# Optimization experiments

Hardware: AMD Instinct MI355X
Metric: run time of the kernel (lower is better)

Reference implementation:

```python
import jax, jax.numpy as jnp
import numpy as np

B, N, T, D, H = 8, 1000, 64, 32, 4
HD = D // H
GEN_INTERVAL = 5.0


def setup_inputs() -> dict:
    key = jax.random.key(0)
    ks = jax.random.split(key, 10)
    s = 1.0 / np.sqrt(D)
    inp = {
        "x": jax.random.normal(ks[0], (B, N, T, D), dtype=jnp.float32),
        "q_w": jax.random.uniform(ks[1], (D, D), jnp.float32, -s, s),
        "q_b": jnp.zeros((D,), jnp.float32),
        "k_w": jax.random.uniform(ks[2], (D, D), jnp.float32, -s, s),
        "k_b": jnp.zeros((D,), jnp.float32),
        "v_w": jax.random.uniform(ks[3], (D, D), jnp.float32, -s, s),
        "v_b": jnp.zeros((D,), jnp.float32),
        "out_w": jax.random.uniform(ks[4], (D, D), jnp.float32, -s, s),
        "out_b": jnp.zeros((D,), jnp.float32),
        "rel_pos_bias": jax.random.uniform(ks[5], (H, T, T), jnp.float32, -s, s),
        "log_gi": jnp.array(np.log(GEN_INTERVAL), jnp.float32),
    }
    return inp


def _gi_mask(log_gi, t):
    # generation-interval weighting: gaussian around gen_int + recency term, causal
    gen_int = jnp.exp(log_gi)
    times = jnp.arange(t, dtype=jnp.float32)
    lag = times[:, None] - times[None, :]  # [T, T]
    weight = jnp.exp(-0.5 * ((lag - gen_int) / (gen_int * 0.5)) ** 2)
    recent = jnp.exp(-0.1 * jnp.abs(lag))
    mask = 0.7 * weight + 0.3 * recent
    causal = jnp.tril(jnp.ones((t, t), jnp.float32))
    return mask * causal


def reference(x, q_w, q_b, k_w, k_b, v_w, v_b, out_w, out_b, rel_pos_bias, log_gi):
    b, n, t, d = x.shape
    xf = x.reshape(b * n, t, d)
    q = (xf @ q_w + q_b).reshape(b * n, t, H, HD).transpose(0, 2, 1, 3)  # [BN,H,T,hd]
    k = (xf @ k_w + k_b).reshape(b * n, t, H, HD).transpose(0, 2, 1, 3)
    v = (xf @ v_w + v_b).reshape(b * n, t, H, HD).transpose(0, 2, 1, 3)
    scale = jnp.sqrt(jnp.asarray(HD, jnp.float32))
    attn = jnp.einsum("bhqd,bhkd->bhqk", q, k) / scale  # [BN,H,T,T]
    attn = attn + rel_pos_bias[None]
    gi = _gi_mask(log_gi, t)
    attn = attn * gi[None, None]
    attn = jax.nn.softmax(attn, axis=-1)
    out = jnp.einsum("bhqk,bhkd->bhqd", attn, v)
    out = out.transpose(0, 2, 1, 3).reshape(b * n, t, d)
    out = out @ out_w + out_b
    return out.reshape(b, n, t, d)
```

## Files before the change

kernel.cpp:

```cpp
#include <hip/hip_runtime.h>
#include <math.h>

namespace {
constexpr int T_ = 64;
constexpr int D_ = 32;

typedef _Float16 half2 __attribute__((ext_vector_type(2)));
typedef _Float16 half4 __attribute__((ext_vector_type(4)));
typedef _Float16 half8 __attribute__((ext_vector_type(8)));
typedef float f32x4 __attribute__((ext_vector_type(4)));

union H4 { half4 v4; half2 v2[2]; };

__global__ __launch_bounds__(256) void gia_prep(
    const float* __restrict__ qw, const float* __restrict__ kw,
    const float* __restrict__ vw, const float* __restrict__ ow,
    const float* __restrict__ rel, const float* __restrict__ lgi,
    float* __restrict__ gis32, _Float16* __restrict__ ebg,
    _Float16* __restrict__ wimg)
{
    int t = blockIdx.x * 256 + threadIdx.x;
    const float gv = __expf(lgi[0]);
    const float LOG2E = 1.4426950408889634f;
    const float INVS  = 0.35355339059327373f;
    if (t < 1024) {
        int nt = t >> 8, mt = (t >> 6) & 3, lane = t & 63;
        int q  = (lane & 15) + 16 * nt;
        int k0 = 16 * mt + 4 * (lane >> 4);
#pragma unroll
        for (int r = 0; r < 4; ++r) {
            int k = k0 + r;
            float gi = 0.0f;
            if (k <= q) {
                float lag = (float)(q - k);
                float z = (lag - gv) / (0.5f * gv);
                gi = 0.7f * __expf(-0.5f * z * z) + 0.3f * __expf(-0.1f * lag);
            }
            gis32[t * 4 + r] = gi * INVS * LOG2E;
        }
    } else if (t < 5120) {
        int e = t - 1024;
        int h = e >> 10, nt = (e >> 8) & 3, mt = (e >> 6) & 3, lane = e & 63;
        int q  = (lane & 15) + 16 * nt;
        int k0 = 16 * mt + 4 * (lane >> 4);
#pragma unroll
        for (int r = 0; r < 4; ++r) {
            int k = k0 + r;
            float gi = 0.0f;
            if (k <= q) {
                float lag = (float)(q - k);
                float z = (lag - gv) / (0.5f * gv);
                gi = 0.7f * __expf(-0.5f * z * z) + 0.3f * __expf(-0.1f * lag);
            }
            ebg[e * 4 + r] = (_Float16)__expf(rel[(h * 64 + q) * 64 + k] * gi);
        }
    } else if (t < 7424) {
        int wi = t - 5120;
        const float* wp[4] = {qw, kw, vw, ow};
#pragma unroll
        for (int e = 0; e < 2; ++e) {
            int flat = wi * 2 + e;
            int m = flat / 1152, rem = flat % 1152;
            int c2 = rem / 36, kk = rem % 36;
            float v = (kk < 32) ? wp[m][kk * 32 + c2] : 0.0f;
            wimg[flat] = (_Float16)v;
        }
    }
}

__global__ __launch_bounds__(256) void gia_main(
    const float* __restrict__ x,
    const float* __restrict__ qb_, const float* __restrict__ kb_,
    const float* __restrict__ vb_, const float* __restrict__ ob_,
    const float* __restrict__ gis32, const _Float16* __restrict__ ebg,
    const _Float16* __restrict__ wimg,
    float* __restrict__ out)
{
    __shared__ __align__(16) _Float16 xs[64][40];
    __shared__ __align__(16) _Float16 wS[4][32][36];
    __shared__ __align__(16) _Float16 qs[64][40];
    __shared__ __align__(16) _Float16 ks_[64][40];
    __shared__ __align__(16) _Float16 vT[37][72];
    __shared__ float bS[4][32];
    __shared__ float invS[4][64];

    const int tid  = threadIdx.x;
    const int lane = tid & 63;
    const int w    = tid >> 6;
    const int l4   = lane & 15;
    const int g    = lane >> 4;
    const int bn   = blockIdx.x;

    {
        const float4* xv = (const float4*)(x + (size_t)bn * 2048);
        float4 a = xv[2 * tid], b = xv[2 * tid + 1];
        int t = tid >> 2, c = (tid & 3) * 8;
        half8 hx;
        hx[0] = (_Float16)a.x; hx[1] = (_Float16)a.y;
        hx[2] = (_Float16)a.z; hx[3] = (_Float16)a.w;
        hx[4] = (_Float16)b.x; hx[5] = (_Float16)b.y;
        hx[6] = (_Float16)b.z; hx[7] = (_Float16)b.w;
        *(half8*)&xs[t][c] = hx;

        const uint4* wsrc = (const uint4*)wimg;
        uint4* wdst = (uint4*)&wS[0][0][0];
        wdst[tid]       = wsrc[tid];
        wdst[tid + 256] = wsrc[tid + 256];
        if (tid < 64) wdst[tid + 512] = wsrc[tid + 512];

        if (tid < 128) {
            int h = tid >> 5, j = tid & 31;
            half2 o2 = {(_Float16)1.0f, (_Float16)1.0f};
            *(half2*)&vT[9 * h + 8][2 * j] = o2;
        }
        if (tid < 128) {
            int m = tid >> 5, i = tid & 31;
            const float* bp = (m == 0) ? qb_ : (m == 1) ? kb_ : (m == 2) ? vb_ : ob_;
            bS[m][i] = bp[i];
        }
    }
    __syncthreads();

    {
        half4 xa0 = *(const half4*)&xs[16 * w + l4][4 * g];
        half4 xa1 = *(const half4*)&xs[16 * w + l4][4 * g + 16];
#pragma unroll
        for (int m = 0; m < 3; ++m) {
#pragma unroll
            for (int nt = 0; nt < 2; ++nt) {
                half4 wb0 = *(const half4*)&wS[m][l4 + 16 * nt][4 * g];
                half4 wb1 = *(const half4*)&wS[m][l4 + 16 * nt][4 * g + 16];
                f32x4 acc = {};
                acc = __builtin_amdgcn_mfma_f32_16x16x16f16(xa0, wb0, acc, 0, 0, 0);
                acc = __builtin_amdgcn_mfma_f32_16x16x16f16(xa1, wb1, acc, 0, 0, 0);
                float bb = bS[m][l4 + 16 * nt];
                if (m == 0) {
#pragma unroll
                    for (int r = 0; r < 4; ++r)
                        qs[g * 4 + r + 16 * w][l4 + 16 * nt] = (_Float16)(acc[r] + bb);
                } else if (m == 1) {
#pragma unroll
                    for (int r = 0; r < 4; ++r)
                        ks_[g * 4 + r + 16 * w][l4 + 16 * nt] = (_Float16)(acc[r] + bb);
                } else {
                    half4 pv;
#pragma unroll
                    for (int r = 0; r < 4; ++r) pv[r] = (_Float16)(acc[r] + bb);
                    int c = l4 + 16 * nt;
                    *(half4*)&vT[9 * (c >> 3) + (c & 7)][g * 4 + 16 * w] = pv;
                }
            }
        }
    }
    __syncthreads();

    {
        const int h = w;
        half4 kfr[4], qfr[4], vfr[4];
#pragma unroll
        for (int mt = 0; mt < 4; ++mt) {
            half4 v = {};
            if (g < 2) v = *(const half4*)&ks_[l4 + 16 * mt][8 * h + 4 * g];
            kfr[mt] = v;
        }
#pragma unroll
        for (int nt = 0; nt < 4; ++nt) {
            half4 v = {};
            if (g < 2) v = *(const half4*)&qs[l4 + 16 * nt][8 * h + 4 * g];
            qfr[nt] = v;
        }
        const int vrow = 9 * h + (l4 < 9 ? l4 : 9);
#pragma unroll
        for (int ks = 0; ks < 4; ++ks)
            vfr[ks] = *(const half4*)&vT[vrow][4 * g + 16 * ks];

        f32x4 oacc[4];
#pragma unroll
        for (int i = 0; i < 4; ++i) oacc[i] = (f32x4){};

#pragma unroll
        for (int nt = 0; nt < 4; ++nt) {
            f32x4 s[4];
#pragma unroll
            for (int mt = 0; mt < 4; ++mt) {
                f32x4 z = {};
                s[mt] = __builtin_amdgcn_mfma_f32_16x16x16f16(kfr[mt], qfr[nt], z, 0, 0, 0);
            }
            half4 af[4];
#pragma unroll
            for (int mt = 0; mt < 4; ++mt) {
                f32x4 g4 = *(const f32x4*)&gis32[((nt * 4 + mt) * 64 + lane) * 4];
                half4 eb = *(const half4*)&ebg[(((h * 4 + nt) * 4 + mt) * 64 + lane) * 4];
                float t0 = s[mt][0] * g4[0];
                float t1 = s[mt][1] * g4[1];
                float t2 = s[mt][2] * g4[2];
                float t3 = s[mt][3] * g4[3];
                H4 u;
                u.v2[0] = __builtin_bit_cast(half2, __builtin_amdgcn_cvt_pkrtz(exp2f(t0), exp2f(t1)));
                u.v2[1] = __builtin_bit_cast(half2, __builtin_amdgcn_cvt_pkrtz(exp2f(t2), exp2f(t3)));
                af[mt] = u.v4 * eb;
            }
#pragma unroll
            for (int ks = 0; ks < 4; ++ks)
                oacc[nt] = __builtin_amdgcn_mfma_f32_16x16x16f16(af[ks], vfr[ks], oacc[nt], 0, 0, 0);
        }

        _Float16 (*os_)[40] = xs;
        if (l4 < 8) {
#pragma unroll
            for (int nt = 0; nt < 4; ++nt)
#pragma unroll
                for (int r = 0; r < 4; ++r)
                    os_[g * 4 + r + 16 * nt][8 * h + l4] = (_Float16)oacc[nt][r];
        } else if (l4 == 8) {
#pragma unroll
            for (int nt = 0; nt < 4; ++nt)
#pragma unroll
                for (int r = 0; r < 4; ++r)
                    invS[h][g * 4 + r + 16 * nt] = oacc[nt][r];
        }
    }
    __syncthreads();

    {
        _Float16 (*os_)[40] = xs;
        half4 oa0 = *(const half4*)&os_[16 * w + l4][4 * g];
        half4 oa1 = *(const half4*)&os_[16 * w + l4][4 * g + 16];
        float i0 = 1.0f / invS[g >> 1][16 * w + l4];
        float i1 = 1.0f / invS[2 + (g >> 1)][16 * w + l4];
        _Float16 h0 = (_Float16)i0, h1 = (_Float16)i1;
        oa0 *= (half4){h0, h0, h0, h0};
        oa1 *= (half4){h1, h1, h1, h1};
        float* yout = out + (size_t)bn * 2048;
#pragma unroll
        for (int nt = 0; nt < 2; ++nt) {
            half4 wb0 = *(const half4*)&wS[3][l4 + 16 * nt][4 * g];
            half4 wb1 = *(const half4*)&wS[3][l4 + 16 * nt][4 * g + 16];
            f32x4 y = {};
            y = __builtin_amdgcn_mfma_f32_16x16x16f16(oa0, wb0, y, 0, 0, 0);
            y = __builtin_amdgcn_mfma_f32_16x16x16f16(oa1, wb1, y, 0, 0, 0);
            float bb = bS[3][l4 + 16 * nt];
#pragma unroll
            for (int r = 0; r < 4; ++r)
                yout[(g * 4 + r + 16 * w) * 32 + l4 + 16 * nt] = y[r] + bb;
        }
    }
}

}

extern "C" void kernel_launch(void* const* d_in, const int* in_sizes, int n_in,
                              void* d_out, int out_size, void* d_ws, size_t ws_size,
                              hipStream_t stream)
{
    const float* x   = (const float*)d_in[0];
    const float* qw  = (const float*)d_in[1];
    const float* qb  = (const float*)d_in[2];
    const float* kw  = (const float*)d_in[3];
    const float* kb  = (const float*)d_in[4];
    const float* vw  = (const float*)d_in[5];
    const float* vb  = (const float*)d_in[6];
    const float* ow  = (const float*)d_in[7];
    const float* ob  = (const float*)d_in[8];
    const float* rel = (const float*)d_in[9];
    const float* lgi = (const float*)d_in[10];
    float* outp = (float*)d_out;

    float*    gis32 = (float*)d_ws;
    _Float16* ebg   = (_Float16*)((char*)d_ws + 16384);
    _Float16* wimg  = (_Float16*)((char*)d_ws + 49152);

    const int bn_count = in_sizes[0] / (T_ * D_);

    gia_prep<<<dim3(29), dim3(256), 0, stream>>>(qw, kw, vw, ow, rel, lgi,
                                                 gis32, ebg, wimg);
    gia_main<<<dim3(bn_count), dim3(256), 0, stream>>>(
        x, qb, kb, vb, ob, gis32, ebg, wimg, outp);
}
```

Measured before the change: 66.14 us.

## Use 16x16x32 MFMA, fold bias into exp2 FMA, shrink LDS for occupancy

Replaces pairs of 16x16x16 f16 MFMAs with single 16x16x32 MFMAs for the projections and output GEMM. The relative-position bias is now precomputed in log2 space as fp32 and fused into the exponent via an FMA, removing the per-element fp16 multiply. The output-projection weights and bias move into registers, shared arrays are trimmed, and launch bounds request 6 blocks per SM. Together these aim to cut LDS footprint and instruction count so more blocks stay resident. The cost is a doubled bias table in global memory and more register pressure.

```diff
diff --git a/kernel.cpp b/kernel.cpp
--- a/kernel.cpp
+++ b/kernel.cpp
@@ -11,12 +11,13 @@
 typedef float f32x4 __attribute__((ext_vector_type(4)));
 
 union H4 { half4 v4; half2 v2[2]; };
+union H8 { half8 v8; half4 v4[2]; };
 
 __global__ __launch_bounds__(256) void gia_prep(
     const float* __restrict__ qw, const float* __restrict__ kw,
     const float* __restrict__ vw, const float* __restrict__ ow,
     const float* __restrict__ rel, const float* __restrict__ lgi,
-    float* __restrict__ gis32, _Float16* __restrict__ ebg,
+    float* __restrict__ gis32, float* __restrict__ lb32,
     _Float16* __restrict__ wimg)
 {
     int t = blockIdx.x * 256 + threadIdx.x;
@@ -52,7 +53,7 @@
                 float z = (lag - gv) / (0.5f * gv);
                 gi = 0.7f * __expf(-0.5f * z * z) + 0.3f * __expf(-0.1f * lag);
             }
-            ebg[e * 4 + r] = (_Float16)__expf(rel[(h * 64 + q) * 64 + k] * gi);
+            lb32[e * 4 + r] = rel[(h * 64 + q) * 64 + k] * gi * LOG2E;
         }
     } else if (t < 7424) {
         int wi = t - 5120;
@@ -68,21 +69,21 @@
     }
 }
 
-__global__ __launch_bounds__(256) void gia_main(
+__global__ __launch_bounds__(256, 6) void gia_main(
     const float* __restrict__ x,
     const float* __restrict__ qb_, const float* __restrict__ kb_,
     const float* __restrict__ vb_, const float* __restrict__ ob_,
-    const float* __restrict__ gis32, const _Float16* __restrict__ ebg,
+    const float* __restrict__ gis32, const float* __restrict__ lb32,
     const _Float16* __restrict__ wimg,
     float* __restrict__ out)
 {
     __shared__ __align__(16) _Float16 xs[64][40];
-    __shared__ __align__(16) _Float16 wS[4][32][36];
-    __shared__ __align__(16) _Float16 qs[64][40];
-    __shared__ __align__(16) _Float16 ks_[64][40];
-    __shared__ __align__(16) _Float16 vT[37][72];
-    __shared__ float bS[4][32];
-    __shared__ float invS[4][64];
+    __shared__ __align__(16) _Float16 wS[3][32][36];
+    __shared__ __align__(16) _Float16 qs[64][36];
+    __shared__ __align__(16) _Float16 ks_[64][36];
+    __shared__ __align__(16) _Float16 vT[36][68];
+    __shared__ float bS[3][32];
+    __shared__ _Float16 invS[4][64];
 
     const int tid  = threadIdx.x;
     const int lane = tid & 63;
@@ -90,6 +91,15 @@
     const int l4   = lane & 15;
     const int g    = lane >> 4;
     const int bn   = blockIdx.x;
+
+    H8 wo[2]; float obv[2];
+#pragma unroll
+    for (int nt = 0; nt < 2; ++nt) {
+        const _Float16* wp = wimg + 3 * 1152 + (l4 + 16 * nt) * 36 + 8 * g;
+        wo[nt].v4[0] = *(const half4*)wp;
+        wo[nt].v4[1] = *(const half4*)(wp + 4);
+        obv[nt] = ob_[l4 + 16 * nt];
+    }
 
     {
         const float4* xv = (const float4*)(x + (size_t)bn * 2048);
@@ -104,35 +114,33 @@
 
         const uint4* wsrc = (const uint4*)wimg;
         uint4* wdst = (uint4*)&wS[0][0][0];
-        wdst[tid]       = wsrc[tid];
-        wdst[tid + 256] = wsrc[tid + 256];
-        if (tid < 64) wdst[tid + 512] = wsrc[tid + 512];
+        wdst[tid] = wsrc[tid];
+        if (tid < 176) wdst[tid + 256] = wsrc[tid + 256];
 
         if (tid < 128) {
             int h = tid >> 5, j = tid & 31;
             half2 o2 = {(_Float16)1.0f, (_Float16)1.0f};
             *(half2*)&vT[9 * h + 8][2 * j] = o2;
         }
-        if (tid < 128) {
+        if (tid < 96) {
             int m = tid >> 5, i = tid & 31;
-            const float* bp = (m == 0) ? qb_ : (m == 1) ? kb_ : (m == 2) ? vb_ : ob_;
+            const float* bp = (m == 0) ? qb_ : (m == 1) ? kb_ : vb_;
             bS[m][i] = bp[i];
         }
     }
     __syncthreads();
 
     {
-        half4 xa0 = *(const half4*)&xs[16 * w + l4][4 * g];
-        half4 xa1 = *(const half4*)&xs[16 * w + l4][4 * g + 16];
+        half8 xa = *(const half8*)&xs[16 * w + l4][8 * g];
 #pragma unroll
         for (int m = 0; m < 3; ++m) {
 #pragma unroll
             for (int nt = 0; nt < 2; ++nt) {
-                half4 wb0 = *(const half4*)&wS[m][l4 + 16 * nt][4 * g];
-                half4 wb1 = *(const half4*)&wS[m][l4 + 16 * nt][4 * g + 16];
+                H8 wb;
+                wb.v4[0] = *(const half4*)&wS[m][l4 + 16 * nt][8 * g];
+                wb.v4[1] = *(const half4*)&wS[m][l4 + 16 * nt][8 * g + 4];
                 f32x4 acc = {};
-                acc = __builtin_amdgcn_mfma_f32_16x16x16f16(xa0, wb0, acc, 0, 0, 0);
-                acc = __builtin_amdgcn_mfma_f32_16x16x16f16(xa1, wb1, acc, 0, 0, 0);
+                acc = __builtin_amdgcn_mfma_f32_16x16x32_f16(xa, wb.v8, acc, 0, 0, 0);
                 float bb = bS[m][l4 + 16 * nt];
                 if (m == 0) {
 #pragma unroll
@@ -169,7 +177,7 @@
             if (g < 2) v = *(const half4*)&qs[l4 + 16 * nt][8 * h + 4 * g];
             qfr[nt] = v;
         }
-        const int vrow = 9 * h + (l4 < 9 ? l4 : 9);
+        const int vrow = 9 * h + (l4 < 9 ? l4 : 8);
 #pragma unroll
         for (int ks = 0; ks < 4; ++ks)
             vfr[ks] = *(const half4*)&vT[vrow][4 * g + 16 * ks];
@@ -189,16 +197,16 @@
             half4 af[4];
 #pragma unroll
             for (int mt = 0; mt < 4; ++mt) {
-                f32x4 g4 = *(const f32x4*)&gis32[((nt * 4 + mt) * 64 + lane) * 4];
-                half4 eb = *(const half4*)&ebg[(((h * 4 + nt) * 4 + mt) * 64 + lane) * 4];
-                float t0 = s[mt][0] * g4[0];
-                float t1 = s[mt][1] * g4[1];
-                float t2 = s[mt][2] * g4[2];
-                float t3 = s[mt][3] * g4[3];
+                f32x4 g4  = *(const f32x4*)&gis32[((nt * 4 + mt) * 64 + lane) * 4];
+                f32x4 lbv = *(const f32x4*)&lb32[(((h * 4 + nt) * 4 + mt) * 64 + lane) * 4];
+                float t0 = fmaf(s[mt][0], g4[0], lbv[0]);
+                float t1 = fmaf(s[mt][1], g4[1], lbv[1]);
+                float t2 = fmaf(s[mt][2], g4[2], lbv[2]);
+                float t3 = fmaf(s[mt][3], g4[3], lbv[3]);
                 H4 u;
                 u.v2[0] = __builtin_bit_cast(half2, __builtin_amdgcn_cvt_pkrtz(exp2f(t0), exp2f(t1)));
                 u.v2[1] = __builtin_bit_cast(half2, __builtin_amdgcn_cvt_pkrtz(exp2f(t2), exp2f(t3)));
-                af[mt] = u.v4 * eb;
+                af[mt] = u.v4;
             }
 #pragma unroll
             for (int ks = 0; ks < 4; ++ks)
@@ -217,32 +225,28 @@
             for (int nt = 0; nt < 4; ++nt)
 #pragma unroll
                 for (int r = 0; r < 4; ++r)
-                    invS[h][g * 4 + r + 16 * nt] = oacc[nt][r];
+                    invS[h][g * 4 + r + 16 * nt] = (_Float16)oacc[nt][r];
         }
     }
     __syncthreads();
 
     {
         _Float16 (*os_)[40] = xs;
-        half4 oa0 = *(const half4*)&os_[16 * w + l4][4 * g];
-        half4 oa1 = *(const half4*)&os_[16 * w + l4][4 * g + 16];
-        float i0 = 1.0f / invS[g >> 1][16 * w + l4];
-        float i1 = 1.0f / invS[2 + (g >> 1)][16 * w + l4];
-        _Float16 h0 = (_Float16)i0, h1 = (_Float16)i1;
-        oa0 *= (half4){h0, h0, h0, h0};
-        oa1 *= (half4){h1, h1, h1, h1};
+        half4 o0 = *(const half4*)&os_[16 * w + l4][8 * g];
+        half4 o1 = *(const half4*)&os_[16 * w + l4][8 * g + 4];
+        float iv = 1.0f / (float)invS[g][16 * w + l4];
+        _Float16 hv = (_Float16)iv;
+        o0 *= (half4){hv, hv, hv, hv};
+        o1 *= (half4){hv, hv, hv, hv};
+        H8 oa; oa.v4[0] = o0; oa.v4[1] = o1;
         float* yout = out + (size_t)bn * 2048;
 #pragma unroll
         for (int nt = 0; nt < 2; ++nt) {
-            half4 wb0 = *(const half4*)&wS[3][l4 + 16 * nt][4 * g];
-            half4 wb1 = *(const half4*)&wS[3][l4 + 16 * nt][4 * g + 16];
             f32x4 y = {};
-            y = __builtin_amdgcn_mfma_f32_16x16x16f16(oa0, wb0, y, 0, 0, 0);
-            y = __builtin_amdgcn_mfma_f32_16x16x16f16(oa1, wb1, y, 0, 0, 0);
-            float bb = bS[3][l4 + 16 * nt];
+            y = __builtin_amdgcn_mfma_f32_16x16x32_f16(oa.v8, wo[nt].v8, y, 0, 0, 0);
 #pragma unroll
             for (int r = 0; r < 4; ++r)
-                yout[(g * 4 + r + 16 * w) * 32 + l4 + 16 * nt] = y[r] + bb;
+                yout[(g * 4 + r + 16 * w) * 32 + l4 + 16 * nt] = y[r] + obv[nt];
         }
     }
 }
@@ -267,13 +271,13 @@
     float* outp = (float*)d_out;
 
     float*    gis32 = (float*)d_ws;
-    _Float16* ebg   = (_Float16*)((char*)d_ws + 16384);
-    _Float16* wimg  = (_Float16*)((char*)d_ws + 49152);
+    float*    lb32  = (float*)((char*)d_ws + 16384);
+    _Float16* wimg  = (_Float16*)((char*)d_ws + 81920);
 
     const int bn_count = in_sizes[0] / (T_ * D_);
 
     gia_prep<<<dim3(29), dim3(256), 0, stream>>>(qw, kw, vw, ow, rel, lgi,
-                                                 gis32, ebg, wimg);
+                                                 gis32, lb32, wimg);
     gia_main<<<dim3(bn_count), dim3(256), 0, stream>>>(
-        x, qb, kb, vb, ob, gis32, ebg, wimg, outp);
-}
+        x, qb, kb, vb, ob, gis32, lb32, wimg, outp);
+}
```

Measured after the change: 65.63 us. About the same (-0.8%).
